# Performance work log

Measured on AMD Instinct MI355X. Metric: run time of the kernel, lower is better.

Reference implementation:

```python
import jax, jax.numpy as jnp
import numpy as np

NUM_HEADS = 8


def setup_inputs() -> dict:
    key = jax.random.key(0)
    ks = jax.random.split(key, 16)
    B, C = 4, 512
    size = (8, 16, 16)
    def w(k):
        return jax.random.normal(k, (C, C), dtype=jnp.float32) * 0.02
    z = lambda: jnp.zeros((C,), jnp.float32)
    return {
        'x1': jax.random.normal(ks[0], (B, C) + size, dtype=jnp.float32),
        'x2': jax.random.normal(ks[1], (B, C) + size, dtype=jnp.float32),
        'Wq': w(ks[2]), 'bq': z(),
        'Wk': w(ks[3]), 'bk': z(),
        'Wv1': w(ks[4]), 'bv1': z(),
        'Wv2': w(ks[5]), 'bv2': z(),
        'Wo1': w(ks[6]), 'bo1': z(),
        'Wo2': w(ks[7]), 'bo2': z(),
    }


def reference(x1, x2, Wq, bq, Wk, bk, Wv1, bv1, Wv2, bv2, Wo1, bo1, Wo2, bo2):
    B, C = x1.shape[:2]
    size = x1.shape[2:]              # spatial dims, e.g. (8,16,16)
    N = int(np.prod(size))           # tokens
    dh = C // NUM_HEADS
    # flatten spatial -> (B, N, C)
    h1 = x1.reshape(B, C, N).transpose(0, 2, 1)
    h2 = x2.reshape(B, C, N).transpose(0, 2, 1)

    def heads(x):                    # (B,N,C) -> (B,H,N,dh)
        return x.reshape(B, N, NUM_HEADS, dh).transpose(0, 2, 1, 3)

    q = heads(h1 @ Wq + bq)
    k = heads(h2 @ Wk + bk)
    v1 = heads(h1 @ Wv1 + bv1)
    v2 = heads(h2 @ Wv2 + bv2)

    scores = jnp.einsum('bhqd,bhkd->bhqk', q, k) / jnp.sqrt(jnp.float32(dh))
    p1 = jax.nn.softmax(scores, axis=-2)                      # normalize over queries
    p2 = jnp.swapaxes(jax.nn.softmax(scores, axis=-1), -1, -2)  # (B,H,Nk,Nq)

    ctx1 = jnp.einsum('bhqk,bhkd->bhqd', p1, v1)
    ctx2 = jnp.einsum('bhkq,bhqd->bhkd', p2, v2)

    def merge(ctx):                  # (B,H,N,dh) -> (B,N,C)
        return ctx.transpose(0, 2, 1, 3).reshape(B, N, C)

    o1 = (merge(ctx1) @ Wo1 + bo1).transpose(0, 2, 1).reshape((B, C) + size) + x1
    o2 = (merge(ctx2) @ Wo2 + bo2).transpose(0, 2, 1).reshape((B, C) + size) + x2
    return (o1, o2)
```

## Files before the change

### kernel.cpp

```cpp
#include <hip/hip_runtime.h>

typedef __attribute__((ext_vector_type(8))) __bf16 bf16x8;
typedef __attribute__((ext_vector_type(4))) float f32x4;
typedef __attribute__((ext_vector_type(16))) float f32x16;
typedef unsigned int u32;

#define MFMA32(a, b, c) __builtin_amdgcn_mfma_f32_32x32x16_bf16((a), (b), (c), 0, 0, 0)
#define EXP2(x) __builtin_amdgcn_exp2f(x)
#define SETPRIO(n) __builtin_amdgcn_s_setprio(n)

static constexpr int Bsz = 4, C = 512, N = 2048, H = 8, DH = 64;
static constexpr int BN = Bsz * N;
static constexpr size_t BCN = (size_t)Bsz * C * N;
static constexpr float SM_C = 0.18033688011112042f;

__device__ __forceinline__ void gload16(const void* g, void* lds) {
  __builtin_amdgcn_global_load_lds(
      (const __attribute__((address_space(1))) u32*)g,
      (__attribute__((address_space(3))) u32*)lds, 16, 0, 0);
}

__device__ __forceinline__ u32 cvt_pk_bf16(float lo, float hi) {
  u32 r;
  asm("v_cvt_pk_bf16_f32 %0, %1, %2" : "=v"(r) : "v"(lo), "v"(hi));
  return r;
}

__device__ __forceinline__ void permswap32(u32& a, u32& b) {
  asm volatile("v_permlane32_swap_b32 %0, %1" : "+v"(a), "+v"(b));
}

static constexpr size_t SZ_BF = (size_t)BN * C * sizeof(__bf16);
static constexpr size_t SZ_W  = (size_t)C * C * sizeof(__bf16);
static constexpr size_t SZ_ST = (size_t)Bsz * H * N * sizeof(float);
static constexpr size_t OFF_HT1  = 0;
static constexpr size_t OFF_HT2  = OFF_HT1 + SZ_BF;
static constexpr size_t OFF_Q    = OFF_HT2 + SZ_BF;
static constexpr size_t OFF_K    = OFF_Q + SZ_BF;
static constexpr size_t OFF_VT1  = OFF_K + SZ_BF;
static constexpr size_t OFF_VT2  = OFF_VT1 + SZ_BF;
static constexpr size_t OFF_CTX1 = OFF_VT2 + SZ_BF;
static constexpr size_t OFF_CTX2 = OFF_CTX1 + SZ_BF;
static constexpr size_t OFF_WQT  = OFF_CTX2 + SZ_BF;
static constexpr size_t OFF_WKT  = OFF_WQT + SZ_W;
static constexpr size_t OFF_WV1T = OFF_WKT + SZ_W;
static constexpr size_t OFF_WV2T = OFF_WV1T + SZ_W;
static constexpr size_t OFF_WO1T = OFF_WV2T + SZ_W;
static constexpr size_t OFF_WO2T = OFF_WO1T + SZ_W;
static constexpr size_t OFF_QS   = OFF_WO2T + SZ_W;
static constexpr size_t OFF_KS   = OFF_QS + SZ_ST;

__global__ __launch_bounds__(256) void k_tc2(const float* __restrict__ x1,
                                             const float* __restrict__ x2,
                                             __bf16* __restrict__ h1,
                                             __bf16* __restrict__ h2) {
  __shared__ __bf16 tile[64][66];
  int z = blockIdx.z;
  size_t boff = (size_t)(z & 3) * C * N;
  const float* src = (z < 4 ? x1 : x2) + boff;
  __bf16* dst = (z < 4 ? h1 : h2) + boff;
  int r0 = blockIdx.y * 64, c0 = blockIdx.x * 64;
  int t = threadIdx.x;
  int cl = t & 63, rr = t >> 6;
#pragma unroll
  for (int i = 0; i < 16; ++i) {
    int r = rr * 16 + i;
    tile[r][cl] = (__bf16)src[(size_t)(r0 + r) * N + c0 + cl];
  }
  __syncthreads();
#pragma unroll
  for (int i = 0; i < 16; ++i) {
    int c = rr * 16 + i;
    dst[(size_t)(c0 + c) * C + r0 + cl] = tile[cl][c];
  }
}

struct WT6 {
  const float* src[6];
  __bf16* dst[6];
};
__global__ __launch_bounds__(256) void k_tcw(WT6 p) {
  __shared__ __bf16 tile[64][66];
  int z = blockIdx.z;
  const float* src = p.src[z];
  __bf16* dst = p.dst[z];
  int r0 = blockIdx.y * 64, c0 = blockIdx.x * 64;
  int t = threadIdx.x;
  int cl = t & 63, rr = t >> 6;
#pragma unroll
  for (int i = 0; i < 16; ++i) {
    int r = rr * 16 + i;
    tile[r][cl] = (__bf16)src[(size_t)(r0 + r) * C + c0 + cl];
  }
  __syncthreads();
#pragma unroll
  for (int i = 0; i < 16; ++i) {
    int c = rr * 16 + i;
    dst[(size_t)(c0 + c) * C + r0 + cl] = tile[cl][c];
  }
}

struct GArgs {
  const __bf16* A; const __bf16* Bt; const float* bias; const float* rs;
  __bf16* outb; float* outf; const float* resid; float scale;
};

template <int MODE>
__global__ __launch_bounds__(256, 2) void k_gemm(GArgs g0, GArgs g1) {
  __shared__ __bf16 As[2 * 128 * 64];
  __shared__ __bf16 Bs[2 * 128 * 64];
  int lin = blockIdx.x;
  int swz = (lin & 7) * 64 + (lin >> 3);
  int dir = swz >> 8;
  int inner = swz & 255;
  const __bf16* Ap = dir ? g1.A : g0.A;
  const __bf16* Bp = dir ? g1.Bt : g0.Bt;
  const float* bias = dir ? g1.bias : g0.bias;
  const float* rs = dir ? g1.rs : g0.rs;
  __bf16* outb = dir ? g1.outb : g0.outb;
  float* outf = dir ? g1.outf : g0.outf;
  const float* resid = dir ? g1.resid : g0.resid;
  float scale = dir ? g1.scale : g0.scale;
  int m0 = (inner & 63) * 128, n0 = (inner >> 6) * 128;
  int t = threadIdx.x, lane = t & 63, w = t >> 6;
  int wm = w >> 1, wn = w & 1;
  int l31 = lane & 31, hi = lane >> 5;
  int srow = t >> 3;
  int sc8 = ((t & 7) ^ (srow & 7)) * 8;
  int swA = (l31 & 7) << 4;
  f32x16 acc[2][2] = {};

#define GSTAGE(p, k0)                                                        \
  {                                                                          \
    _Pragma("unroll") for (int gI = 0; gI < 4; ++gI) {                       \
      int row_ = gI * 32 + srow;                                             \
      gload16(&Ap[(size_t)(m0 + row_) * C + (k0) + sc8],                     \
              (char*)As + (p) * 16384 + gI * 4096 + w * 1024);               \
      gload16(&Bp[(size_t)(n0 + row_) * C + (k0) + sc8],                     \
              (char*)Bs + (p) * 16384 + gI * 4096 + w * 1024);               \
    }                                                                        \
  }

  GSTAGE(0, 0)
  __syncthreads();
  for (int ks = 0; ks < 8; ++ks) {
    int p = ks & 1;
    if (ks < 7) GSTAGE(p ^ 1, (ks + 1) * 64)
    const char* ab = (const char*)As + p * 16384;
    const char* bb = (const char*)Bs + p * 16384;
#pragma unroll
    for (int kk = 0; kk < 4; ++kk) {
      int ko = (kk * 32 + hi * 16);
      bf16x8 a0 = *(const bf16x8*)(ab + (wm * 64 + l31) * 128 + (ko ^ swA));
      bf16x8 a1 = *(const bf16x8*)(ab + (wm * 64 + 32 + l31) * 128 + (ko ^ swA));
      bf16x8 b0 = *(const bf16x8*)(bb + (wn * 64 + l31) * 128 + (ko ^ swA));
      bf16x8 b1 = *(const bf16x8*)(bb + (wn * 64 + 32 + l31) * 128 + (ko ^ swA));
      acc[0][0] = MFMA32(a0, b0, acc[0][0]);
      acc[0][1] = MFMA32(a0, b1, acc[0][1]);
      acc[1][0] = MFMA32(a1, b0, acc[1][0]);
      acc[1][1] = MFMA32(a1, b1, acc[1][1]);
    }
    __syncthreads();
  }
#pragma unroll
  for (int mi = 0; mi < 2; ++mi)
#pragma unroll
    for (int ni = 0; ni < 2; ++ni) {
      int gn = n0 + wn * 64 + ni * 32 + l31;
      float bv = bias[gn];
#pragma unroll
      for (int g2 = 0; g2 < 4; ++g2) {
        int gm = m0 + wm * 64 + mi * 32 + 8 * g2 + 4 * hi;
        int b = gm >> 11, n = gm & 2047;
        if (MODE == 0) {
          int h = gn >> 6, d = gn & 63;
          size_t base = (size_t)(b * 8 + h) * 2048 + n;
#pragma unroll
          for (int j = 0; j < 4; ++j)
            outb[(base + j) * 64 + d] = (__bf16)((acc[mi][ni][4 * g2 + j] + bv) * scale);
        } else if (MODE == 1) {
          int h = gn >> 6, d = gn & 63;
          size_t tok = (size_t)(b * 8 + h) * 2048 + n;
          float4 sv = *reinterpret_cast<const float4*>(&rs[tok]);
          size_t addr = ((size_t)(b * 8 + h) * 64 + d) * 2048 + n;
          union { __bf16 h4[4]; uint2 u; } pk;
          pk.h4[0] = (__bf16)((acc[mi][ni][4 * g2 + 0] + bv) * __builtin_amdgcn_rcpf(sv.x));
          pk.h4[1] = (__bf16)((acc[mi][ni][4 * g2 + 1] + bv) * __builtin_amdgcn_rcpf(sv.y));
          pk.h4[2] = (__bf16)((acc[mi][ni][4 * g2 + 2] + bv) * __builtin_amdgcn_rcpf(sv.z));
          pk.h4[3] = (__bf16)((acc[mi][ni][4 * g2 + 3] + bv) * __builtin_amdgcn_rcpf(sv.w));
          *reinterpret_cast<uint2*>(&outb[addr]) = pk.u;
        } else {
          size_t addr = ((size_t)b * C + gn) * 2048 + n;
          float4 xv = *reinterpret_cast<const float4*>(&resid[addr]);
          float4 ov;
          ov.x = acc[mi][ni][4 * g2 + 0] + bv + xv.x;
          ov.y = acc[mi][ni][4 * g2 + 1] + bv + xv.y;
          ov.z = acc[mi][ni][4 * g2 + 2] + bv + xv.z;
          ov.w = acc[mi][ni][4 * g2 + 3] + bv + xv.w;
          *reinterpret_cast<float4*>(&outf[addr]) = ov;
        }
      }
    }
}

struct SArgs { const __bf16* X; const __bf16* Y; float* ors; };

__global__ __launch_bounds__(256, 2) void k_stats(SArgs sa0, SArgs sa1) {
  __shared__ __bf16 Ys[2 * 64 * 64];
  int lin = blockIdx.x;
  int swz = (lin & 7) * 64 + (lin >> 3);
  int dir = swz >> 8;
  int inner = swz & 255;
  const __bf16* X = dir ? sa1.X : sa0.X;
  const __bf16* Y = dir ? sa1.Y : sa0.Y;
  float* ors = dir ? sa1.ors : sa0.ors;
  int bh = inner >> 3, xblk = inner & 7;
  int t = threadIdx.x, lane = t & 63, w = t >> 6;
  int l31 = lane & 31, hi = lane >> 5;
  const __bf16* Xb = X + (size_t)bh * N * DH;
  const __bf16* Yb = Y + (size_t)bh * N * DH;
  int qg = xblk * 256 + w * 64 + l31;
  bf16x8 xq[2][4];
#pragma unroll
  for (int s = 0; s < 2; ++s)
#pragma unroll
    for (int kk = 0; kk < 4; ++kk)
      xq[s][kk] = *(const bf16x8*)&Xb[(size_t)(qg + s * 32) * DH + kk * 16 + hi * 8];
  int srow = t >> 3;
  int sc8 = ((t & 7) ^ (srow & 7)) * 8;
#define SSTAGE(p, kc2)                                                       \
  {                                                                          \
    char* yb_ = (char*)Ys + (p) * 8192 + w * 1024;                           \
    gload16(&Yb[(size_t)((kc2) + srow) * DH + sc8], yb_);                    \
    gload16(&Yb[(size_t)((kc2) + 32 + srow) * DH + sc8], yb_ + 4096);        \
  }
  float sum0 = 0.f, sum1 = 0.f;
  SSTAGE(0, 0)
  __syncthreads();
  for (int it = 0; it < 32; ++it) {
    int p = it & 1;
    if (it < 31) SSTAGE(p ^ 1, (it + 1) * 64)
    const char* yb = (const char*)Ys + p * 8192;
#pragma unroll
    for (int cblk = 0; cblk < 2; ++cblk) {
      f32x16 s0 = {}, s1 = {};
      int row = cblk * 32 + l31;
      int sw = (row & 7) << 4;
      SETPRIO(1);
#pragma unroll
      for (int kk = 0; kk < 4; ++kk) {
        bf16x8 yf = *(const bf16x8*)(yb + row * 128 + ((kk * 32 + hi * 16) ^ sw));
        s0 = MFMA32(yf, xq[0][kk], s0);
        s1 = MFMA32(yf, xq[1][kk], s1);
      }
      SETPRIO(0);
#pragma unroll
      for (int e = 0; e < 16; ++e) {
        sum0 += EXP2(s0[e]);
        sum1 += EXP2(s1[e]);
      }
    }
    __syncthreads();
  }
  sum0 += __shfl_xor(sum0, 32, 64);
  sum1 += __shfl_xor(sum1, 32, 64);
  if (hi == 0) {
    ors[(size_t)bh * N + qg] = sum0;
    ors[(size_t)bh * N + qg + 32] = sum1;
  }
}

struct CArgs { const __bf16* X; const __bf16* Y; const __bf16* Vt; __bf16* out; };

__global__ __launch_bounds__(256, 2) void k_ctx(CArgs c0, CArgs c1) {
  __shared__ __bf16 Ys[2 * 128 * 64];
  __shared__ __bf16 Vs[2 * 64 * 128];
  int lin = blockIdx.x;
  int swz = (lin & 7) * 64 + (lin >> 3);
  int dir = swz >> 8;
  int inner = swz & 255;
  const __bf16* X = dir ? c1.X : c0.X;
  const __bf16* Y = dir ? c1.Y : c0.Y;
  const __bf16* Vt = dir ? c1.Vt : c0.Vt;
  __bf16* out = dir ? c1.out : c0.out;
  int bh = inner >> 3, xblk = inner & 7;
  int b = bh >> 3, h = bh & 7;
  int t = threadIdx.x, lane = t & 63, w = t >> 6;
  int l31 = lane & 31, hi = lane >> 5;
  const __bf16* Xb = X + (size_t)bh * N * DH;
  const __bf16* Yb = Y + (size_t)bh * N * DH;
  const __bf16* Vb = Vt + (size_t)bh * DH * N;
  int qg = xblk * 256 + w * 64 + l31;
  bf16x8 xq[2][4];
#pragma unroll
  for (int s = 0; s < 2; ++s)
#pragma unroll
    for (int kk = 0; kk < 4; ++kk)
      xq[s][kk] = *(const bf16x8*)&Xb[(size_t)(qg + s * 32) * DH + kk * 16 + hi * 8];
  int srow = t >> 3;
  int sc8 = ((t & 7) ^ (srow & 7)) * 8;
  int vrow_s = t >> 4;
  int vc8 = ((t & 15) ^ (vrow_s & 15)) * 8;
#define CSTAGE(p, kc2)                                                        \
  {                                                                           \
    char* yb_ = (char*)Ys + (p) * 16384 + w * 1024;                           \
    char* vb_ = (char*)Vs + (p) * 16384 + w * 1024;                           \
    _Pragma("unroll") for (int gI = 0; gI < 4; ++gI) {                        \
      gload16(&Yb[(size_t)((kc2) + gI * 32 + srow) * DH + sc8],               \
              yb_ + gI * 4096);                                               \
      gload16(&Vb[(size_t)(gI * 16 + vrow_s) * N + (kc2) + vc8],              \
              vb_ + gI * 4096);                                               \
    }                                                                         \
  }
  f32x16 oacc[2][2] = {};
  CSTAGE(0, 0)
  __syncthreads();
  for (int it = 0; it < 16; ++it) {
    int p = it & 1;
    if (it < 15) CSTAGE(p ^ 1, (it + 1) * 128)
    const char* yb = (const char*)Ys + p * 16384;
    const char* vb = (const char*)Vs + p * 16384;
#pragma unroll
    for (int cblk = 0; cblk < 4; ++cblk) {
      f32x16 s0 = {}, s1 = {};
      int row = cblk * 32 + l31;
      int sw = (row & 7) << 4;
      SETPRIO(1);
#pragma unroll
      for (int kk = 0; kk < 4; ++kk) {
        bf16x8 yf = *(const bf16x8*)(yb + row * 128 + ((kk * 32 + hi * 16) ^ sw));
        s0 = MFMA32(yf, xq[0][kk], s0);
        s1 = MFMA32(yf, xq[1][kk], s1);
      }
      SETPRIO(0);
      u32 wl0[4], wh0[4], wl1[4], wh1[4];
#pragma unroll
      for (int g = 0; g < 4; ++g) {
        wl0[g] = cvt_pk_bf16(EXP2(s0[4 * g + 0]), EXP2(s0[4 * g + 1]));
        wh0[g] = cvt_pk_bf16(EXP2(s0[4 * g + 2]), EXP2(s0[4 * g + 3]));
        wl1[g] = cvt_pk_bf16(EXP2(s1[4 * g + 0]), EXP2(s1[4 * g + 1]));
        wh1[g] = cvt_pk_bf16(EXP2(s1[4 * g + 2]), EXP2(s1[4 * g + 3]));
      }
#pragma unroll
      for (int sh = 0; sh < 2; ++sh) {
        int ct = cblk * 2 + sh;
        u32 p00 = wl0[2 * sh], p01 = wl0[2 * sh + 1];
        u32 p02 = wh0[2 * sh], p03 = wh0[2 * sh + 1];
        permswap32(p00, p01);
        permswap32(p02, p03);
        union { u32 wd[4]; bf16x8 v; } pf0;
        pf0.wd[0] = p00; pf0.wd[1] = p02; pf0.wd[2] = p01; pf0.wd[3] = p03;
        u32 p10 = wl1[2 * sh], p11 = wl1[2 * sh + 1];
        u32 p12 = wh1[2 * sh], p13 = wh1[2 * sh + 1];
        permswap32(p10, p11);
        permswap32(p12, p13);
        union { u32 wd[4]; bf16x8 v; } pf1;
        pf1.wd[0] = p10; pf1.wd[1] = p12; pf1.wd[2] = p11; pf1.wd[3] = p13;
        SETPRIO(1);
#pragma unroll
        for (int dblk = 0; dblk < 2; ++dblk) {
          int vrow = dblk * 32 + l31;
          int vw = (vrow & 15) << 4;
          bf16x8 vf = *(const bf16x8*)(vb + vrow * 256 + ((ct * 32 + hi * 16) ^ vw));
          oacc[0][dblk] = MFMA32(vf, pf0.v, oacc[0][dblk]);
          oacc[1][dblk] = MFMA32(vf, pf1.v, oacc[1][dblk]);
        }
        SETPRIO(0);
      }
    }
    __syncthreads();
  }
#pragma unroll
  for (int s = 0; s < 2; ++s)
#pragma unroll
    for (int dblk = 0; dblk < 2; ++dblk)
#pragma unroll
      for (int g = 0; g < 4; ++g) {
        union { __bf16 h4[4]; uint2 u; } pk;
#pragma unroll
        for (int m = 0; m < 4; ++m) pk.h4[m] = (__bf16)oacc[s][dblk][4 * g + m];
        int d = dblk * 32 + 8 * g + 4 * hi;
        size_t addr = ((size_t)b * N + qg + s * 32) * C + h * 64 + d;
        *reinterpret_cast<uint2*>(&out[addr]) = pk.u;
      }
}

extern "C" void kernel_launch(void* const* d_in, const int* in_sizes, int n_in,
                              void* d_out, int out_size, void* d_ws, size_t ws_size,
                              hipStream_t stream) {
  (void)in_sizes; (void)n_in; (void)out_size; (void)ws_size;
  const float* x1  = (const float*)d_in[0];
  const float* x2  = (const float*)d_in[1];
  const float* Wq  = (const float*)d_in[2];
  const float* bq  = (const float*)d_in[3];
  const float* Wk  = (const float*)d_in[4];
  const float* bk  = (const float*)d_in[5];
  const float* Wv1 = (const float*)d_in[6];
  const float* bv1 = (const float*)d_in[7];
  const float* Wv2 = (const float*)d_in[8];
  const float* bv2 = (const float*)d_in[9];
  const float* Wo1 = (const float*)d_in[10];
  const float* bo1 = (const float*)d_in[11];
  const float* Wo2 = (const float*)d_in[12];
  const float* bo2 = (const float*)d_in[13];

  char* ws = (char*)d_ws;
  __bf16* ht1  = (__bf16*)(ws + OFF_HT1);
  __bf16* ht2  = (__bf16*)(ws + OFF_HT2);
  __bf16* qb   = (__bf16*)(ws + OFF_Q);
  __bf16* kb   = (__bf16*)(ws + OFF_K);
  __bf16* vt1  = (__bf16*)(ws + OFF_VT1);
  __bf16* vt2  = (__bf16*)(ws + OFF_VT2);
  __bf16* ctx1 = (__bf16*)(ws + OFF_CTX1);
  __bf16* ctx2 = (__bf16*)(ws + OFF_CTX2);
  __bf16* wqt  = (__bf16*)(ws + OFF_WQT);
  __bf16* wkt  = (__bf16*)(ws + OFF_WKT);
  __bf16* wv1t = (__bf16*)(ws + OFF_WV1T);
  __bf16* wv2t = (__bf16*)(ws + OFF_WV2T);
  __bf16* wo1t = (__bf16*)(ws + OFF_WO1T);
  __bf16* wo2t = (__bf16*)(ws + OFF_WO2T);
  float* qs = (float*)(ws + OFF_QS);
  float* ks = (float*)(ws + OFF_KS);
  float* outf = (float*)d_out;

  dim3 blk(256);
  k_tc2<<<dim3(32, 8, 8), blk, 0, stream>>>(x1, x2, ht1, ht2);
  WT6 wt;
  wt.src[0] = Wq;  wt.dst[0] = wqt;
  wt.src[1] = Wk;  wt.dst[1] = wkt;
  wt.src[2] = Wv1; wt.dst[2] = wv1t;
  wt.src[3] = Wv2; wt.dst[3] = wv2t;
  wt.src[4] = Wo1; wt.dst[4] = wo1t;
  wt.src[5] = Wo2; wt.dst[5] = wo2t;
  k_tcw<<<dim3(8, 8, 6), blk, 0, stream>>>(wt);

  GArgs gq0{ht1, wqt, bq, nullptr, qb, nullptr, nullptr, SM_C};
  GArgs gq1{ht2, wkt, bk, nullptr, kb, nullptr, nullptr, 1.0f};
  k_gemm<0><<<512, blk, 0, stream>>>(gq0, gq1);

  SArgs st0{qb, kb, qs};
  SArgs st1{kb, qb, ks};
  k_stats<<<512, blk, 0, stream>>>(st0, st1);

  GArgs gv0{ht1, wv1t, bv1, ks, vt1, nullptr, nullptr, 0.f};
  GArgs gv1{ht2, wv2t, bv2, qs, vt2, nullptr, nullptr, 0.f};
  k_gemm<1><<<512, blk, 0, stream>>>(gv0, gv1);

  CArgs cc0{qb, kb, vt1, ctx1};
  CArgs cc1{kb, qb, vt2, ctx2};
  k_ctx<<<512, blk, 0, stream>>>(cc0, cc1);

  GArgs go0{ctx1, wo1t, bo1, nullptr, nullptr, outf, x1, 0.f};
  GArgs go1{ctx2, wo2t, bo2, nullptr, nullptr, outf + BCN, x2, 0.f};
  k_gemm<2><<<512, blk, 0, stream>>>(go0, go1);
}
```

Before: 191.4 us.

## Halve per-block query tile in stats/ctx kernels, double grid, prefetch GEMM LDS fragments

The stats and ctx attention kernels now handle 32 queries per wave instead of 64, giving 128 queries per block and 1024 blocks. The ctx kernel's K/V staging tile shrinks from 128 to 64 keys. Launch bounds rise to 6 and 4 blocks per CU so more waves are resident. The GEMM inner loop also software-pipelines its LDS fragment loads one k-step ahead of the MFMAs. The cost is that each K/V tile is reused by fewer queries, so total K/V traffic roughly doubles.

```diff
diff --git a/kernel.cpp b/kernel.cpp
--- a/kernel.cpp
+++ b/kernel.cpp
@@ -128,6 +128,10 @@
   int srow = t >> 3;
   int sc8 = ((t & 7) ^ (srow & 7)) * 8;
   int swA = (l31 & 7) << 4;
+  int aoff0 = (wm * 64 + l31) * 128;
+  int aoff1 = (wm * 64 + 32 + l31) * 128;
+  int boff0 = (wn * 64 + l31) * 128;
+  int boff1 = (wn * 64 + 32 + l31) * 128;
   f32x16 acc[2][2] = {};
 
 #define GSTAGE(p, k0)                                                        \
@@ -148,17 +152,26 @@
     if (ks < 7) GSTAGE(p ^ 1, (ks + 1) * 64)
     const char* ab = (const char*)As + p * 16384;
     const char* bb = (const char*)Bs + p * 16384;
+    int ko0 = (hi * 16) ^ swA;
+    bf16x8 a0c = *(const bf16x8*)(ab + aoff0 + ko0);
+    bf16x8 a1c = *(const bf16x8*)(ab + aoff1 + ko0);
+    bf16x8 b0c = *(const bf16x8*)(bb + boff0 + ko0);
+    bf16x8 b1c = *(const bf16x8*)(bb + boff1 + ko0);
 #pragma unroll
     for (int kk = 0; kk < 4; ++kk) {
-      int ko = (kk * 32 + hi * 16);
-      bf16x8 a0 = *(const bf16x8*)(ab + (wm * 64 + l31) * 128 + (ko ^ swA));
-      bf16x8 a1 = *(const bf16x8*)(ab + (wm * 64 + 32 + l31) * 128 + (ko ^ swA));
-      bf16x8 b0 = *(const bf16x8*)(bb + (wn * 64 + l31) * 128 + (ko ^ swA));
-      bf16x8 b1 = *(const bf16x8*)(bb + (wn * 64 + 32 + l31) * 128 + (ko ^ swA));
-      acc[0][0] = MFMA32(a0, b0, acc[0][0]);
-      acc[0][1] = MFMA32(a0, b1, acc[0][1]);
-      acc[1][0] = MFMA32(a1, b0, acc[1][0]);
-      acc[1][1] = MFMA32(a1, b1, acc[1][1]);
+      bf16x8 a0n, a1n, b0n, b1n;
+      if (kk < 3) {
+        int ko = ((kk + 1) * 32 + hi * 16) ^ swA;
+        a0n = *(const bf16x8*)(ab + aoff0 + ko);
+        a1n = *(const bf16x8*)(ab + aoff1 + ko);
+        b0n = *(const bf16x8*)(bb + boff0 + ko);
+        b1n = *(const bf16x8*)(bb + boff1 + ko);
+      }
+      acc[0][0] = MFMA32(a0c, b0c, acc[0][0]);
+      acc[0][1] = MFMA32(a0c, b1c, acc[0][1]);
+      acc[1][0] = MFMA32(a1c, b0c, acc[1][0]);
+      acc[1][1] = MFMA32(a1c, b1c, acc[1][1]);
+      if (kk < 3) { a0c = a0n; a1c = a1n; b0c = b0n; b1c = b1n; }
     }
     __syncthreads();
   }
@@ -205,36 +218,36 @@
 
 struct SArgs { const __bf16* X; const __bf16* Y; float* ors; };
 
-__global__ __launch_bounds__(256, 2) void k_stats(SArgs sa0, SArgs sa1) {
+__global__ __launch_bounds__(256, 6) void k_stats(SArgs sa0, SArgs sa1) {
   __shared__ __bf16 Ys[2 * 64 * 64];
   int lin = blockIdx.x;
-  int swz = (lin & 7) * 64 + (lin >> 3);
-  int dir = swz >> 8;
-  int inner = swz & 255;
+  int swz = (lin & 7) * 128 + (lin >> 3);
+  int dir = swz >> 9;
+  int inner = swz & 511;
   const __bf16* X = dir ? sa1.X : sa0.X;
   const __bf16* Y = dir ? sa1.Y : sa0.Y;
   float* ors = dir ? sa1.ors : sa0.ors;
-  int bh = inner >> 3, xblk = inner & 7;
+  int bh = inner >> 4, xblk = inner & 15;
   int t = threadIdx.x, lane = t & 63, w = t >> 6;
   int l31 = lane & 31, hi = lane >> 5;
   const __bf16* Xb = X + (size_t)bh * N * DH;
   const __bf16* Yb = Y + (size_t)bh * N * DH;
-  int qg = xblk * 256 + w * 64 + l31;
-  bf16x8 xq[2][4];
-#pragma unroll
-  for (int s = 0; s < 2; ++s)
-#pragma unroll
-    for (int kk = 0; kk < 4; ++kk)
-      xq[s][kk] = *(const bf16x8*)&Xb[(size_t)(qg + s * 32) * DH + kk * 16 + hi * 8];
+  int qg = xblk * 128 + w * 32 + l31;
+  bf16x8 xq[4];
+#pragma unroll
+  for (int kk = 0; kk < 4; ++kk)
+    xq[kk] = *(const bf16x8*)&Xb[(size_t)qg * DH + kk * 16 + hi * 8];
   int srow = t >> 3;
   int sc8 = ((t & 7) ^ (srow & 7)) * 8;
+  int ybase = l31 * 128;
+  int sw = (l31 & 7) << 4;
 #define SSTAGE(p, kc2)                                                       \
   {                                                                          \
     char* yb_ = (char*)Ys + (p) * 8192 + w * 1024;                           \
     gload16(&Yb[(size_t)((kc2) + srow) * DH + sc8], yb_);                    \
     gload16(&Yb[(size_t)((kc2) + 32 + srow) * DH + sc8], yb_ + 4096);        \
   }
-  float sum0 = 0.f, sum1 = 0.f;
+  float sa_ = 0.f, sb_ = 0.f;
   SSTAGE(0, 0)
   __syncthreads();
   for (int it = 0; it < 32; ++it) {
@@ -243,103 +256,90 @@
     const char* yb = (const char*)Ys + p * 8192;
 #pragma unroll
     for (int cblk = 0; cblk < 2; ++cblk) {
-      f32x16 s0 = {}, s1 = {};
-      int row = cblk * 32 + l31;
-      int sw = (row & 7) << 4;
+      f32x16 s0 = {};
       SETPRIO(1);
 #pragma unroll
       for (int kk = 0; kk < 4; ++kk) {
-        bf16x8 yf = *(const bf16x8*)(yb + row * 128 + ((kk * 32 + hi * 16) ^ sw));
-        s0 = MFMA32(yf, xq[0][kk], s0);
-        s1 = MFMA32(yf, xq[1][kk], s1);
+        bf16x8 yf = *(const bf16x8*)(yb + cblk * 4096 + ybase +
+                                     ((kk * 32 + hi * 16) ^ sw));
+        s0 = MFMA32(yf, xq[kk], s0);
       }
       SETPRIO(0);
 #pragma unroll
-      for (int e = 0; e < 16; ++e) {
-        sum0 += EXP2(s0[e]);
-        sum1 += EXP2(s1[e]);
+      for (int e = 0; e < 8; ++e) {
+        sa_ += EXP2(s0[e]);
+        sb_ += EXP2(s0[e + 8]);
       }
     }
     __syncthreads();
   }
+  float sum0 = sa_ + sb_;
   sum0 += __shfl_xor(sum0, 32, 64);
-  sum1 += __shfl_xor(sum1, 32, 64);
-  if (hi == 0) {
-    ors[(size_t)bh * N + qg] = sum0;
-    ors[(size_t)bh * N + qg + 32] = sum1;
-  }
+  if (hi == 0) ors[(size_t)bh * N + qg] = sum0;
 }
 
 struct CArgs { const __bf16* X; const __bf16* Y; const __bf16* Vt; __bf16* out; };
 
-__global__ __launch_bounds__(256, 2) void k_ctx(CArgs c0, CArgs c1) {
-  __shared__ __bf16 Ys[2 * 128 * 64];
-  __shared__ __bf16 Vs[2 * 64 * 128];
+__global__ __launch_bounds__(256, 4) void k_ctx(CArgs c0, CArgs c1) {
+  __shared__ __bf16 Ys[2 * 64 * 64];
+  __shared__ __bf16 Vs[2 * 64 * 64];
   int lin = blockIdx.x;
-  int swz = (lin & 7) * 64 + (lin >> 3);
-  int dir = swz >> 8;
-  int inner = swz & 255;
+  int swz = (lin & 7) * 128 + (lin >> 3);
+  int dir = swz >> 9;
+  int inner = swz & 511;
   const __bf16* X = dir ? c1.X : c0.X;
   const __bf16* Y = dir ? c1.Y : c0.Y;
   const __bf16* Vt = dir ? c1.Vt : c0.Vt;
   __bf16* out = dir ? c1.out : c0.out;
-  int bh = inner >> 3, xblk = inner & 7;
+  int bh = inner >> 4, xblk = inner & 15;
   int b = bh >> 3, h = bh & 7;
   int t = threadIdx.x, lane = t & 63, w = t >> 6;
   int l31 = lane & 31, hi = lane >> 5;
   const __bf16* Xb = X + (size_t)bh * N * DH;
   const __bf16* Yb = Y + (size_t)bh * N * DH;
   const __bf16* Vb = Vt + (size_t)bh * DH * N;
-  int qg = xblk * 256 + w * 64 + l31;
-  bf16x8 xq[2][4];
-#pragma unroll
-  for (int s = 0; s < 2; ++s)
-#pragma unroll
-    for (int kk = 0; kk < 4; ++kk)
-      xq[s][kk] = *(const bf16x8*)&Xb[(size_t)(qg + s * 32) * DH + kk * 16 + hi * 8];
+  int qg = xblk * 128 + w * 32 + l31;
+  bf16x8 xq[4];
+#pragma unroll
+  for (int kk = 0; kk < 4; ++kk)
+    xq[kk] = *(const bf16x8*)&Xb[(size_t)qg * DH + kk * 16 + hi * 8];
   int srow = t >> 3;
   int sc8 = ((t & 7) ^ (srow & 7)) * 8;
-  int vrow_s = t >> 4;
-  int vc8 = ((t & 15) ^ (vrow_s & 15)) * 8;
+  int ybase = l31 * 128;
+  int sw = (l31 & 7) << 4;
 #define CSTAGE(p, kc2)                                                        \
   {                                                                           \
-    char* yb_ = (char*)Ys + (p) * 16384 + w * 1024;                           \
-    char* vb_ = (char*)Vs + (p) * 16384 + w * 1024;                           \
-    _Pragma("unroll") for (int gI = 0; gI < 4; ++gI) {                        \
-      gload16(&Yb[(size_t)((kc2) + gI * 32 + srow) * DH + sc8],               \
-              yb_ + gI * 4096);                                               \
-      gload16(&Vb[(size_t)(gI * 16 + vrow_s) * N + (kc2) + vc8],              \
-              vb_ + gI * 4096);                                               \
-    }                                                                         \
-  }
-  f32x16 oacc[2][2] = {};
+    char* yb_ = (char*)Ys + (p) * 8192 + w * 1024;                            \
+    char* vb_ = (char*)Vs + (p) * 8192 + w * 1024;                            \
+    gload16(&Yb[(size_t)((kc2) + srow) * DH + sc8], yb_);                     \
+    gload16(&Yb[(size_t)((kc2) + 32 + srow) * DH + sc8], yb_ + 4096);         \
+    gload16(&Vb[(size_t)srow * N + (kc2) + sc8], vb_);                        \
+    gload16(&Vb[(size_t)(32 + srow) * N + (kc2) + sc8], vb_ + 4096);          \
+  }
+  f32x16 oacc[2] = {};
   CSTAGE(0, 0)
   __syncthreads();
-  for (int it = 0; it < 16; ++it) {
+  for (int it = 0; it < 32; ++it) {
     int p = it & 1;
-    if (it < 15) CSTAGE(p ^ 1, (it + 1) * 128)
-    const char* yb = (const char*)Ys + p * 16384;
-    const char* vb = (const char*)Vs + p * 16384;
-#pragma unroll
-    for (int cblk = 0; cblk < 4; ++cblk) {
-      f32x16 s0 = {}, s1 = {};
-      int row = cblk * 32 + l31;
-      int sw = (row & 7) << 4;
+    if (it < 31) CSTAGE(p ^ 1, (it + 1) * 64)
+    const char* yb = (const char*)Ys + p * 8192;
+    const char* vb = (const char*)Vs + p * 8192;
+#pragma unroll
+    for (int cblk = 0; cblk < 2; ++cblk) {
+      f32x16 s0 = {};
       SETPRIO(1);
 #pragma unroll
       for (int kk = 0; kk < 4; ++kk) {
-        bf16x8 yf = *(const bf16x8*)(yb + row * 128 + ((kk * 32 + hi * 16) ^ sw));
-        s0 = MFMA32(yf, xq[0][kk], s0);
-        s1 = MFMA32(yf, xq[1][kk], s1);
+        bf16x8 yf = *(const bf16x8*)(yb + cblk * 4096 + ybase +
+                                     ((kk * 32 + hi * 16) ^ sw));
+        s0 = MFMA32(yf, xq[kk], s0);
       }
       SETPRIO(0);
-      u32 wl0[4], wh0[4], wl1[4], wh1[4];
+      u32 wl0[4], wh0[4];
 #pragma unroll
       for (int g = 0; g < 4; ++g) {
         wl0[g] = cvt_pk_bf16(EXP2(s0[4 * g + 0]), EXP2(s0[4 * g + 1]));
         wh0[g] = cvt_pk_bf16(EXP2(s0[4 * g + 2]), EXP2(s0[4 * g + 3]));
-        wl1[g] = cvt_pk_bf16(EXP2(s1[4 * g + 0]), EXP2(s1[4 * g + 1]));
-        wh1[g] = cvt_pk_bf16(EXP2(s1[4 * g + 2]), EXP2(s1[4 * g + 3]));
       }
 #pragma unroll
       for (int sh = 0; sh < 2; ++sh) {
@@ -350,20 +350,12 @@
         permswap32(p02, p03);
         union { u32 wd[4]; bf16x8 v; } pf0;
         pf0.wd[0] = p00; pf0.wd[1] = p02; pf0.wd[2] = p01; pf0.wd[3] = p03;
-        u32 p10 = wl1[2 * sh], p11 = wl1[2 * sh + 1];
-        u32 p12 = wh1[2 * sh], p13 = wh1[2 * sh + 1];
-        permswap32(p10, p11);
-        permswap32(p12, p13);
-        union { u32 wd[4]; bf16x8 v; } pf1;
-        pf1.wd[0] = p10; pf1.wd[1] = p12; pf1.wd[2] = p11; pf1.wd[3] = p13;
         SETPRIO(1);
 #pragma unroll
         for (int dblk = 0; dblk < 2; ++dblk) {
-          int vrow = dblk * 32 + l31;
-          int vw = (vrow & 15) << 4;
-          bf16x8 vf = *(const bf16x8*)(vb + vrow * 256 + ((ct * 32 + hi * 16) ^ vw));
-          oacc[0][dblk] = MFMA32(vf, pf0.v, oacc[0][dblk]);
-          oacc[1][dblk] = MFMA32(vf, pf1.v, oacc[1][dblk]);
+          bf16x8 vf = *(const bf16x8*)(vb + (dblk * 32 + l31) * 128 +
+                                       ((ct * 32 + hi * 16) ^ sw));
+          oacc[dblk] = MFMA32(vf, pf0.v, oacc[dblk]);
         }
         SETPRIO(0);
       }
@@ -371,18 +363,16 @@
     __syncthreads();
   }
 #pragma unroll
-  for (int s = 0; s < 2; ++s)
-#pragma unroll
-    for (int dblk = 0; dblk < 2; ++dblk)
-#pragma unroll
-      for (int g = 0; g < 4; ++g) {
-        union { __bf16 h4[4]; uint2 u; } pk;
-#pragma unroll
-        for (int m = 0; m < 4; ++m) pk.h4[m] = (__bf16)oacc[s][dblk][4 * g + m];
-        int d = dblk * 32 + 8 * g + 4 * hi;
-        size_t addr = ((size_t)b * N + qg + s * 32) * C + h * 64 + d;
-        *reinterpret_cast<uint2*>(&out[addr]) = pk.u;
-      }
+  for (int dblk = 0; dblk < 2; ++dblk)
+#pragma unroll
+    for (int g = 0; g < 4; ++g) {
+      union { __bf16 h4[4]; uint2 u; } pk;
+#pragma unroll
+      for (int m = 0; m < 4; ++m) pk.h4[m] = (__bf16)oacc[dblk][4 * g + m];
+      int d = dblk * 32 + 8 * g + 4 * hi;
+      size_t addr = ((size_t)b * N + qg) * C + h * 64 + d;
+      *reinterpret_cast<uint2*>(&out[addr]) = pk.u;
+    }
 }
 
 extern "C" void kernel_launch(void* const* d_in, const int* in_sizes, int n_in,
@@ -440,7 +430,7 @@
 
   SArgs st0{qb, kb, qs};
   SArgs st1{kb, qb, ks};
-  k_stats<<<512, blk, 0, stream>>>(st0, st1);
+  k_stats<<<1024, blk, 0, stream>>>(st0, st1);
 
   GArgs gv0{ht1, wv1t, bv1, ks, vt1, nullptr, nullptr, 0.f};
   GArgs gv1{ht2, wv2t, bv2, qs, vt2, nullptr, nullptr, 0.f};
@@ -448,7 +438,7 @@
 
   CArgs cc0{qb, kb, vt1, ctx1};
   CArgs cc1{kb, qb, vt2, ctx2};
-  k_ctx<<<512, blk, 0, stream>>>(cc0, cc1);
+  k_ctx<<<1024, blk, 0, stream>>>(cc0, cc1);
 
   GArgs go0{ctx1, wo1t, bo1, nullptr, nullptr, outf, x1, 0.f};
   GArgs go1{ctx2, wo2t, bo2, nullptr, nullptr, outf + BCN, x2, 0.f};
```

Result: no change. 192.7 us (+0.7%).
